# Performance work log

Hardware: AMD Instinct MI355X
Metric: run time of the kernel (lower is better)

Reference implementation:

```python
import jax, jax.numpy as jnp
import numpy as np

B, S, E = 8, 2048, 768
N, H = 12, 64
INIT = 0.02
IGNORE = -100000.0


def setup_inputs() -> dict:
    key = jax.random.key(0)
    ks = jax.random.split(key, 5)
    return {
        "normalized_resid_pre": jax.random.normal(ks[0], (B, S, E), jnp.float32),
        "W_Q": jax.random.normal(ks[1], (N, E, H), jnp.float32) * INIT,
        "W_K": jax.random.normal(ks[2], (N, E, H), jnp.float32) * INIT,
        "W_V": jax.random.normal(ks[3], (N, E, H), jnp.float32) * INIT,
        "W_O": jax.random.normal(ks[4], (N, H, E), jnp.float32) * INIT,
        "b_Q": jnp.zeros((N, H), jnp.float32),
        "b_K": jnp.zeros((N, H), jnp.float32),
        "b_V": jnp.zeros((N, H), jnp.float32),
        "b_O": jnp.zeros((E,), jnp.float32),
    }


def reference(normalized_resid_pre, W_Q, W_K, W_V, W_O, b_Q, b_K, b_V, b_O):
    x = normalized_resid_pre
    b, s, e = x.shape
    d_head = W_Q.shape[-1]
    q = jnp.einsum('bse,neh->bsnh', x, W_Q) + b_Q  # [b, sq, n, h]
    k = jnp.einsum('bse,neh->bsnh', x, W_K) + b_K
    v = jnp.einsum('bse,neh->bsnh', x, W_V) + b_V
    scores = jnp.einsum('bqnh,bknh->bnqk', q, k) / jnp.sqrt(jnp.float32(d_head))
    mask = jnp.tril(jnp.ones((s, s), jnp.float32))  # [sq, sk]
    masked = mask * scores + (1.0 - mask) * IGNORE
    probs = jax.nn.softmax(masked, axis=-1)
    z = jnp.einsum('bnqk,bknh->bqnh', probs, v)
    # sum over heads of per-head output projection + bias
    out = jnp.einsum('bqnh,nhe->bqe', z, W_O) + b_O
    return out
```

## Files before the change

### kernel.cpp

```cpp
#include <hip/hip_runtime.h>
#include <hip/hip_bf16.h>
#include <stdint.h>


#define B_ 8
#define S_ 2048
#define E_ 768
#define NHEADS 12
#define HD 64
#define BS (B_*S_)
#define NHD (NHEADS*HD)

typedef short bf16x8 __attribute__((ext_vector_type(8)));
typedef short bf16x4 __attribute__((ext_vector_type(4)));
typedef float f32x4  __attribute__((ext_vector_type(4)));
typedef __hip_bfloat16 bf16;

typedef const __attribute__((address_space(1))) char* as1_t;
typedef __attribute__((address_space(3))) char* as3_t;

__device__ __forceinline__ f32x4 mfma16(bf16x8 a, bf16x8 b, f32x4 c) {
    return __builtin_amdgcn_mfma_f32_16x16x32_bf16(a, b, c, 0, 0, 0);
}
__device__ __forceinline__ bf16x8 ld8(const bf16* p) {
    return *reinterpret_cast<const bf16x8*>(p);
}
__device__ __forceinline__ void gload16(const bf16* g, bf16* l) {
    __builtin_amdgcn_global_load_lds((as1_t)g, (as3_t)l, 16, 0, 0);
}
__device__ __forceinline__ bf16x8 pack8(f32x4 a, f32x4 b) {
    union { bf16x8 v; __hip_bfloat162 h[4]; } u;
    u.h[0] = __float22bfloat162_rn(make_float2(a[0], a[1]));
    u.h[1] = __float22bfloat162_rn(make_float2(a[2], a[3]));
    u.h[2] = __float22bfloat162_rn(make_float2(b[0], b[1]));
    u.h[3] = __float22bfloat162_rn(make_float2(b[2], b[3]));
    return u.v;
}

__global__ __launch_bounds__(256) void prep_kernel(
    const float* __restrict__ x,  const float* __restrict__ Wq,
    const float* __restrict__ Wk, const float* __restrict__ Wv,
    const float* __restrict__ Wo,
    bf16* __restrict__ xb,  bf16* __restrict__ WqT, bf16* __restrict__ WkT,
    bf16* __restrict__ WvT, bf16* __restrict__ WoT)
{
    const int tid = blockIdx.x * 256 + threadIdx.x;
    const int nth = gridDim.x * 256;
    for (int i = tid; i < BS*E_; i += nth)
        xb[i] = __float2bfloat16(x[i]);
    for (int i = tid; i < NHD*E_; i += nth) {
        const int c = i / E_;
        const int e = i - c*E_;
        const int n = c >> 6, h = c & 63;
        const int src = (n*E_ + e)*HD + h;
        WqT[i] = __float2bfloat16(Wq[src]);
        WkT[i] = __float2bfloat16(Wk[src]);
        WvT[i] = __float2bfloat16(Wv[src]);
        WoT[e*NHD + c] = __float2bfloat16(Wo[i]);
    }
}


#define FENCE() asm volatile("" ::: "memory")
#define VMCNT7() asm volatile("s_waitcnt vmcnt(7)" ::: "memory")
#define MIN11(x) ((x) < 11 ? (x) : 11)

#define A_ELEM(kh, rg) (((kh)*16 + (rg))*512)
#define B_ELEM(kh, rg) (((kh)*12 + (rg))*512)

#define STG_A(dst, gbase, kt, kh) do {                                            \
    const bf16* _s = (gbase) + (size_t)(l16)*768 + (kt)*64 + (kh)*32 + quad*8;    \
    gload16(_s + (size_t)(w*16)*768,     &(dst)[A_ELEM(kh, w)]);                  \
    gload16(_s + (size_t)((w+8)*16)*768, &(dst)[A_ELEM(kh, w+8)]);                \
} while (0)

#define STG_B(dst, gbase, kt) do {                                                \
    const bf16* _s = (gbase) + (size_t)(l16)*768 + (kt)*64 + quad*8;              \
    const int _k1 = (w < 4) ? 0 : 1;                                              \
    const int _r1 = (w < 4) ? (w + 8) : (w - 4);                                  \
    gload16(_s + (size_t)(w*16)*768,        &(dst)[B_ELEM(0, w)]);                \
    gload16(_s + (size_t)(_r1*16)*768 + _k1*32, &(dst)[B_ELEM(_k1, _r1)]);        \
    gload16(_s + (size_t)((w+4)*16)*768 + 32,   &(dst)[B_ELEM(1, w+4)]);          \
} while (0)

#define PHASE(bufA, bufB, q, LOADB, STAGE, WAIT) do {                             \
    if (LOADB) {                                                                  \
        _Pragma("unroll") for (int n = 0; n < 3; ++n)                             \
        _Pragma("unroll") for (int ks = 0; ks < 2; ++ks)                          \
            bfr[n][ks] = ld8(&(bufB)[((ks)*12 + wn*3 + n)*512 + lane*8]);         \
    }                                                                             \
    bf16x8 afr[2][2];                                                             \
    _Pragma("unroll") for (int m = 0; m < 2; ++m)                                 \
    _Pragma("unroll") for (int ks = 0; ks < 2; ++ks)                              \
        afr[m][ks] = ld8(&(bufA)[((ks)*16 + wm*8 + (q)*2 + m)*512 + lane*8]);     \
    STAGE;                                                                        \
    FENCE(); __builtin_amdgcn_s_barrier(); FENCE();                               \
    asm volatile("s_waitcnt lgkmcnt(0)" ::: "memory");                            \
    __builtin_amdgcn_s_setprio(1);                                                \
    _Pragma("unroll") for (int m = 0; m < 2; ++m)                                 \
    _Pragma("unroll") for (int n = 0; n < 3; ++n)                                 \
    _Pragma("unroll") for (int ks = 0; ks < 2; ++ks)                              \
        acc[(q)*2 + m][n] = mfma16(afr[m][ks], bfr[n][ks], acc[(q)*2 + m][n]);    \
    __builtin_amdgcn_s_setprio(0);                                                \
    WAIT;                                                                         \
    FENCE(); __builtin_amdgcn_s_barrier(); FENCE();                               \
} while (0)

#define ITER8(r0, r1, w2, k0, Ab, Bb)                                             \
    PHASE(r0, sB0, 0, 1, STG_A(w2, Ab, MIN11((k0)+2), 0), (void)0);               \
    PHASE(r0, sB0, 1, 0, STG_A(w2, Ab, MIN11((k0)+2), 1), (void)0);               \
    PHASE(r0, sB0, 2, 0, STG_B(sB0, Bb, MIN11((k0)+2)),   (void)0);               \
    PHASE(r0, sB0, 3, 0, (void)0,                         VMCNT7());              \
    PHASE(r1, sB1, 0, 1, STG_A(r0, Ab, MIN11((k0)+3), 0), (void)0);               \
    PHASE(r1, sB1, 1, 0, STG_A(r0, Ab, MIN11((k0)+3), 1), (void)0);               \
    PHASE(r1, sB1, 2, 0, STG_B(sB1, Bb, MIN11((k0)+3)),   (void)0);               \
    PHASE(r1, sB1, 3, 0, (void)0,                         VMCNT7());

#define GEMM192_BODY(Ab, Bb)                                                      \
    f32x4 acc[8][3];                                                              \
    _Pragma("unroll") for (int mf = 0; mf < 8; ++mf)                              \
    _Pragma("unroll") for (int nf = 0; nf < 3; ++nf)                              \
        acc[mf][nf] = (f32x4){0.f, 0.f, 0.f, 0.f};                                \
    bf16x8 bfr[3][2];                                                             \
    STG_A(sA0, Ab, 0, 0); STG_A(sA0, Ab, 0, 1);                                   \
    STG_B(sB0, Bb, 0);                                                            \
    STG_A(sA1, Ab, 1, 0); STG_A(sA1, Ab, 1, 1);                                   \
    STG_B(sB1, Bb, 1);                                                            \
    VMCNT7();                                                                     \
    FENCE(); __builtin_amdgcn_s_barrier(); FENCE();                               \
    _Pragma("unroll 1")                                                           \
    for (int ii = 0; ii < 2; ++ii) {                                              \
        const int k0 = 6*ii;                                                      \
        ITER8(sA0, sA1, sA2, k0+0, Ab, Bb)                                        \
        ITER8(sA2, sA0, sA1, k0+2, Ab, Bb)                                        \
        ITER8(sA1, sA2, sA0, k0+4, Ab, Bb)                                        \
    }                                                                             \
    asm volatile("s_waitcnt vmcnt(0)" ::: "memory");

__global__ __launch_bounds__(512, 2) void qkv_gemm256(
    const bf16* __restrict__ xb, const bf16* __restrict__ WT,
    const float* __restrict__ bq, const float* __restrict__ bk, const float* __restrict__ bv,
    bf16* __restrict__ Qb, bf16* __restrict__ Kb, bf16* __restrict__ VTb)
{
    __shared__ __align__(16) bf16 sA0[16384];
    __shared__ __align__(16) bf16 sA1[16384];
    __shared__ __align__(16) bf16 sA2[16384];
    __shared__ __align__(16) bf16 sB0[12288];
    __shared__ __align__(16) bf16 sB1[12288];

    const int tm = blockIdx.x, tn = blockIdx.y;
    const int lane = threadIdx.x & 63;
    const int w    = threadIdx.x >> 6;
    const int wm = w >> 2, wn = w & 3;
    const int l16 = lane & 15, quad = lane >> 4;
    const bf16* Ab = xb + (size_t)tm*256*E_;
    const bf16* Bb = WT + (size_t)tn*192*E_;

    GEMM192_BODY(Ab, Bb);

    const int mat = tn >> 2;
    const int cloc0 = (tn & 3)*192 + wn*48;
    const float* bias = (mat==0) ? bq : (mat==1) ? bk : bv;
    const float scale = (mat==0) ? 0.125f * 1.44269504088896340736f : 1.0f;
    bf16* dstQK = (mat==0) ? Qb : Kb;
    #pragma unroll
    for (int nf = 0; nf < 3; ++nf) {
        const int col = cloc0 + nf*16 + l16;
        const int hn = col >> 6, h = col & 63;
        const float bb = bias[col];
        #pragma unroll
        for (int mf = 0; mf < 8; ++mf) {
            const int row = tm*256 + wm*128 + mf*16 + quad*4;
            const int bi = row >> 11;
            const int s  = row & (S_-1);
            if (mat < 2) {
                bf16* d = dstQK + ((size_t)(bi*NHEADS + hn)*S_ + s)*HD + h;
                #pragma unroll
                for (int r = 0; r < 4; ++r)
                    d[(size_t)r*HD] = __float2bfloat16((acc[mf][nf][r] + bb)*scale);
            } else {
                bf16* d = VTb + ((size_t)(bi*NHEADS + hn)*HD + h)*S_ + s;
                union { bf16x4 v; bf16 e[4]; } u;
                #pragma unroll
                for (int r = 0; r < 4; ++r) u.e[r] = __float2bfloat16(acc[mf][nf][r] + bb);
                *reinterpret_cast<bf16x4*>(d) = u.v;
            }
        }
    }
}

__global__ __launch_bounds__(512, 2) void out_gemm256(
    const bf16* __restrict__ Z, const bf16* __restrict__ WoT,
    const float* __restrict__ bo, float* __restrict__ out)
{
    __shared__ __align__(16) bf16 sA0[16384];
    __shared__ __align__(16) bf16 sA1[16384];
    __shared__ __align__(16) bf16 sA2[16384];
    __shared__ __align__(16) bf16 sB0[12288];
    __shared__ __align__(16) bf16 sB1[12288];

    const int tm = blockIdx.x, tn = blockIdx.y;
    const int lane = threadIdx.x & 63;
    const int w    = threadIdx.x >> 6;
    const int wm = w >> 2, wn = w & 3;
    const int l16 = lane & 15, quad = lane >> 4;
    const bf16* Ab = Z   + (size_t)tm*256*NHD;
    const bf16* Bb = WoT + (size_t)tn*192*NHD;

    GEMM192_BODY(Ab, Bb);

    #pragma unroll
    for (int nf = 0; nf < 3; ++nf) {
        const int col = tn*192 + wn*48 + nf*16 + l16;
        const float bb = bo[col];
        #pragma unroll
        for (int mf = 0; mf < 8; ++mf) {
            const int row = tm*256 + wm*128 + mf*16 + quad*4;
            float* d = out + (size_t)row*E_ + col;
            #pragma unroll
            for (int r = 0; r < 4; ++r)
                d[(size_t)r*E_] = acc[mf][nf][r] + bb;
        }
    }
}

__global__ __launch_bounds__(256, 3) void attn_kernel(
    const bf16* __restrict__ Qb, const bf16* __restrict__ Kb,
    const bf16* __restrict__ VTb, bf16* __restrict__ Z)
{
    __shared__ __align__(16) bf16 sK[2][64*64];
    __shared__ __align__(16) bf16 sV[2][64*64];

    const int id = blockIdx.x;
    const int bx = id / 96;
    const int g  = id - bx*96;
    const int hn = g % NHEADS, b = g / NHEADS;
    const int tid  = threadIdx.x;
    const int w    = tid >> 6;
    const int lane = tid & 63;
    const int l16 = lane & 15, quad = lane >> 4;
    const size_t bn = (size_t)b*NHEADS + hn;

    const bf16* Qbase = Qb  + bn*S_*HD;
    const bf16* Kbase = Kb  + bn*S_*HD;
    const bf16* Vbase = VTb + bn*HD*S_;

    const int mA = tid, mB = tid + 256;
    const int rA = mA >> 3, cgA = mA & 7;
    const int rB = mB >> 3, cgB = mB & 7;
    const int slA = (rA*8 + ((cgA + rA + (rA>>3)) & 7)) * 8;
    const int slB = (rB*8 + ((cgB + rB + (rB>>3)) & 7)) * 8;
    const size_t vofA = (size_t)rA*S_ + cgA*8;
    const size_t vofB = (size_t)rB*S_ + cgB*8;

    const int kperm = (l16 >> 2)*8 + (l16 & 3);
    int kidx[2][2][2];
    #pragma unroll
    for (int c=0;c<2;c++)
        #pragma unroll
        for (int bg=0;bg<2;bg++)
            #pragma unroll
            for (int hf=0;hf<2;hf++) {
                const int r = 32*c + 4*bg + kperm;
                const int q = hf*4 + quad;
                kidx[c][bg][hf] = (r*8 + ((q + r + (r>>3)) & 7)) * 8;
            }
    int vidx[4][2];
    #pragma unroll
    for (int ht=0;ht<4;ht++)
        #pragma unroll
        for (int c=0;c<2;c++) {
            const int rho = ht*16 + l16;
            const int q = c*4 + quad;
            vidx[ht][c] = (rho*8 + ((q + rho + (rho>>3)) & 7)) * 8;
        }

    #pragma unroll
    for (int half = 0; half < 2; ++half) {
        const int qblk = half ? (S_/128 - 1 - bx) : bx;
        const int ktb  = 2*qblk + 1;
        const int ktw  = 2*qblk + (w >> 1);
        const int qbase = qblk*128 + w*32;

        bf16x8 bqf[2][2];
        #pragma unroll
        for (int qi=0;qi<2;qi++)
            #pragma unroll
            for (int hf=0;hf<2;hf++)
                bqf[qi][hf] = ld8(Qbase + (size_t)(qbase + qi*16 + l16)*HD + hf*32 + quad*8);

        f32x4 acc[2][4];
        #pragma unroll
        for (int qi=0;qi<2;qi++)
            #pragma unroll
            for (int ht=0;ht<4;ht++) acc[qi][ht] = (f32x4){0.f,0.f,0.f,0.f};
        float lsum[2] = {0.f, 0.f};

        bf16x8 k0 = ld8(Kbase + (size_t)mA*8);
        bf16x8 k1 = ld8(Kbase + (size_t)mB*8);
        bf16x8 v0 = ld8(Vbase + vofA);
        bf16x8 v1 = ld8(Vbase + vofB);
        *reinterpret_cast<bf16x8*>(&sK[0][slA]) = k0;
        *reinterpret_cast<bf16x8*>(&sK[0][slB]) = k1;
        *reinterpret_cast<bf16x8*>(&sV[0][slA]) = v0;
        *reinterpret_cast<bf16x8*>(&sV[0][slB]) = v1;
        __syncthreads();

        for (int kt = 0; kt <= ktb; ++kt) {
            if (kt < ktb) {
                const size_t kt1 = (size_t)(kt+1)*64;
                k0 = ld8(Kbase + kt1*HD + (size_t)mA*8);
                k1 = ld8(Kbase + kt1*HD + (size_t)mB*8);
                v0 = ld8(Vbase + vofA + kt1);
                v1 = ld8(Vbase + vofB + kt1);
            }
            if (kt <= ktw) {
                const bf16* kb = sK[kt & 1];
                const bf16* vb = sV[kt & 1];
                #pragma unroll
                for (int c=0;c<2;c++) {
                    const bf16x8 akA0 = ld8(kb + kidx[c][0][0]);
                    const bf16x8 akA1 = ld8(kb + kidx[c][0][1]);
                    const bf16x8 akB0 = ld8(kb + kidx[c][1][0]);
                    const bf16x8 akB1 = ld8(kb + kidx[c][1][1]);
                    bf16x8 av[4];
                    #pragma unroll
                    for (int ht=0;ht<4;ht++) av[ht] = ld8(vb + vidx[ht][c]);

                    #pragma unroll
                    for (int qi=0;qi<2;qi++) {
                        f32x4 s0 = (f32x4){0.f,0.f,0.f,0.f};
                        s0 = mfma16(akA0, bqf[qi][0], s0);
                        s0 = mfma16(akA1, bqf[qi][1], s0);
                        f32x4 s1 = (f32x4){0.f,0.f,0.f,0.f};
                        s1 = mfma16(akB0, bqf[qi][0], s1);
                        s1 = mfma16(akB1, bqf[qi][1], s1);
                        if (kt == ktw) {
                            const int q  = qbase + qi*16 + l16;
                            const int kb0 = kt*64 + c*32 + quad*8;
                            #pragma unroll
                            for (int r=0;r<4;r++) {
                                s0[r] = (kb0 + r     > q) ? -1e30f : s0[r];
                                s1[r] = (kb0 + 4 + r > q) ? -1e30f : s1[r];
                            }
                        }
                        float ls = 0.f;
                        #pragma unroll
                        for (int r=0;r<4;r++) {
                            s0[r] = __builtin_amdgcn_exp2f(s0[r]);
                            s1[r] = __builtin_amdgcn_exp2f(s1[r]);
                            ls += s0[r] + s1[r];
                        }
                        lsum[qi] += ls;
                        const bf16x8 pf = pack8(s0, s1);
                        #pragma unroll
                        for (int ht=0;ht<4;ht++)
                            acc[qi][ht] = mfma16(av[ht], pf, acc[qi][ht]);
                    }
                }
            }
            if (kt < ktb) {
                const int nb = (kt+1) & 1;
                *reinterpret_cast<bf16x8*>(&sK[nb][slA]) = k0;
                *reinterpret_cast<bf16x8*>(&sK[nb][slB]) = k1;
                *reinterpret_cast<bf16x8*>(&sV[nb][slA]) = v0;
                *reinterpret_cast<bf16x8*>(&sV[nb][slB]) = v1;
            }
            __syncthreads();
        }

        #pragma unroll
        for (int qi=0;qi<2;qi++) {
            float rs = lsum[qi];
            rs += __shfl_xor(rs, 16, 64);
            rs += __shfl_xor(rs, 32, 64);
            const float inv_l = 1.0f / rs;
            const int q = qbase + qi*16 + l16;
            bf16* zp = Z + ((size_t)b*S_ + q)*NHD + (size_t)hn*HD + quad*4;
            #pragma unroll
            for (int ht=0;ht<4;ht++) {
                union { bf16x4 v; bf16 e[4]; } u;
                #pragma unroll
                for (int r=0;r<4;r++) u.e[r] = __float2bfloat16(acc[qi][ht][r] * inv_l);
                *reinterpret_cast<bf16x4*>(zp + ht*16) = u.v;
            }
        }
    }
}

extern "C" void kernel_launch(void* const* d_in, const int* in_sizes, int n_in,
                              void* d_out, int out_size, void* d_ws, size_t ws_size,
                              hipStream_t stream)
{
    const float* x  = (const float*)d_in[0];
    const float* Wq = (const float*)d_in[1];
    const float* Wk = (const float*)d_in[2];
    const float* Wv = (const float*)d_in[3];
    const float* Wo = (const float*)d_in[4];
    const float* bq = (const float*)d_in[5];
    const float* bk = (const float*)d_in[6];
    const float* bv = (const float*)d_in[7];
    const float* bo = (const float*)d_in[8];
    float* out = (float*)d_out;

    char* ws = (char*)d_ws;
    size_t off = 0;
    auto alloc = [&](size_t bytes){ char* p = ws + off; off += (bytes + 255) & ~(size_t)255; return p; };
    bf16* xb  = (bf16*)alloc((size_t)BS*E_*2);
    bf16* WT  = (bf16*)alloc((size_t)3*NHD*E_*2);
    bf16* WoT = (bf16*)alloc((size_t)E_*NHD*2);
    bf16* Qb  = (bf16*)alloc((size_t)BS*NHD*2);
    bf16* Kb  = (bf16*)alloc((size_t)BS*NHD*2);
    bf16* VTb = (bf16*)alloc((size_t)BS*NHD*2);
    bf16* Zb  = (bf16*)alloc((size_t)BS*NHD*2);

    bf16* WqT = WT;
    bf16* WkT = WT + (size_t)NHD*E_;
    bf16* WvT = WT + (size_t)2*NHD*E_;

    prep_kernel<<<4096, 256, 0, stream>>>(x, Wq, Wk, Wv, Wo, xb, WqT, WkT, WvT, WoT);
    qkv_gemm256<<<dim3(BS/256, 12), 512, 0, stream>>>(xb, WT, bq, bk, bv, Qb, Kb, VTb);
    attn_kernel<<<768, 256, 0, stream>>>(Qb, Kb, VTb, Zb);
    out_gemm256<<<dim3(BS/256, E_/192), 512, 0, stream>>>(Zb, WoT, bo, out);
}
```

Before: 232.2 us.

## Prepack x and QKV weights into MFMA fragment layout and drop LDS staging

The prep kernel now writes x and the transposed Q/K/V weights in a pre-swizzled 16x32 fragment layout, using vectorized 8-wide conversions for x. A new QKV GEMM with 128x96 tiles and 256 threads loads MFMA operands straight from global memory into registers, with no LDS staging or barriers. This removes shared-memory traffic and synchronization and raises the block count. In exchange it gives up LDS reuse, so each wave rereads operands from global/L2, and there is no explicit software pipelining to hide load latency.

```diff
diff --git a/kernel.cpp b/kernel.cpp
--- a/kernel.cpp
+++ b/kernel.cpp
@@ -37,29 +37,137 @@
     return u.v;
 }
 
+
 __global__ __launch_bounds__(256) void prep_kernel(
     const float* __restrict__ x,  const float* __restrict__ Wq,
     const float* __restrict__ Wk, const float* __restrict__ Wv,
     const float* __restrict__ Wo,
-    bf16* __restrict__ xb,  bf16* __restrict__ WqT, bf16* __restrict__ WkT,
-    bf16* __restrict__ WvT, bf16* __restrict__ WoT)
+    bf16* __restrict__ xp,  bf16* __restrict__ WTp, bf16* __restrict__ WoT)
 {
     const int tid = blockIdx.x * 256 + threadIdx.x;
     const int nth = gridDim.x * 256;
-    for (int i = tid; i < BS*E_; i += nth)
-        xb[i] = __float2bfloat16(x[i]);
+
+    for (int c = tid; c < BS*E_/8; c += nth) {
+        const int r  = c / 96;
+        const int k8 = (c - r*96) * 8;
+        const float4 f0 = *reinterpret_cast<const float4*>(x + (size_t)r*E_ + k8);
+        const float4 f1 = *reinterpret_cast<const float4*>(x + (size_t)r*E_ + k8 + 4);
+        union { bf16x8 v; __hip_bfloat162 h[4]; } u;
+        u.h[0] = __float22bfloat162_rn(make_float2(f0.x, f0.y));
+        u.h[1] = __float22bfloat162_rn(make_float2(f0.z, f0.w));
+        u.h[2] = __float22bfloat162_rn(make_float2(f1.x, f1.y));
+        u.h[3] = __float22bfloat162_rn(make_float2(f1.z, f1.w));
+        const size_t dst = (size_t)((r>>4)*24 + (k8>>5))*512
+                         + (size_t)((((k8>>3)&3)<<4) + (r&15))*8;
+        *reinterpret_cast<bf16x8*>(xp + dst) = u.v;
+    }
+
+    for (int c2 = tid; c2 < NHD*96; c2 += nth) {
+        const int r  = c2 / 96;
+        const int e8 = (c2 - r*96) * 8;
+        const int n = r >> 6, h = r & 63;
+        const float* sq = Wq + (size_t)(n*E_ + e8)*HD + h;
+        const float* sk = Wk + (size_t)(n*E_ + e8)*HD + h;
+        const float* sv = Wv + (size_t)(n*E_ + e8)*HD + h;
+        union { bf16x8 v; bf16 el[8]; } uq, uk, uv;
+        #pragma unroll
+        for (int j = 0; j < 8; ++j) {
+            uq.el[j] = __float2bfloat16(sq[(size_t)j*HD]);
+            uk.el[j] = __float2bfloat16(sk[(size_t)j*HD]);
+            uv.el[j] = __float2bfloat16(sv[(size_t)j*HD]);
+        }
+        const size_t sub = (size_t)(e8>>5)*512
+                         + (size_t)((((e8>>3)&3)<<4) + (r&15))*8;
+        const size_t rg  = (size_t)(r>>4);
+        *reinterpret_cast<bf16x8*>(WTp + ((0*48 + rg)*24)*512 + sub) = uq.v;
+        *reinterpret_cast<bf16x8*>(WTp + ((1*48 + rg)*24)*512 + sub) = uk.v;
+        *reinterpret_cast<bf16x8*>(WTp + ((2*48 + rg)*24)*512 + sub) = uv.v;
+    }
+
     for (int i = tid; i < NHD*E_; i += nth) {
-        const int c = i / E_;
-        const int e = i - c*E_;
-        const int n = c >> 6, h = c & 63;
-        const int src = (n*E_ + e)*HD + h;
-        WqT[i] = __float2bfloat16(Wq[src]);
-        WkT[i] = __float2bfloat16(Wk[src]);
-        WvT[i] = __float2bfloat16(Wv[src]);
-        WoT[e*NHD + c] = __float2bfloat16(Wo[i]);
-    }
-}
-
+        const int cc = i / E_;
+        const int e  = i - cc*E_;
+        WoT[(size_t)e*NHD + cc] = __float2bfloat16(Wo[i]);
+    }
+}
+
+__global__ __launch_bounds__(256, 3) void qkv_gemm_p(
+    const bf16* __restrict__ xp, const bf16* __restrict__ WTp,
+    const float* __restrict__ bq, const float* __restrict__ bk, const float* __restrict__ bv,
+    bf16* __restrict__ Qb, bf16* __restrict__ Kb, bf16* __restrict__ VTb)
+{
+    const int tm = blockIdx.x, tn = blockIdx.y;
+    const int lane = threadIdx.x & 63;
+    const int w    = threadIdx.x >> 6;
+    const int wm = w >> 1, wn = w & 1;
+    const int l16 = lane & 15, quad = lane >> 4;
+    const bf16* Abase = xp  + (size_t)(tm*8 + wm*4)*24*512 + lane*8;
+    const bf16* Bbase = WTp + (size_t)(tn*6 + wn*3)*24*512 + lane*8;
+
+    f32x4 acc[4][3];
+    #pragma unroll
+    for (int mf = 0; mf < 4; ++mf)
+        #pragma unroll
+        for (int nf = 0; nf < 3; ++nf)
+            acc[mf][nf] = (f32x4){0.f, 0.f, 0.f, 0.f};
+
+    #pragma unroll
+    for (int kt = 0; kt < 12; ++kt) {
+        bf16x8 af[4][2], bfr[3][2];
+        #pragma unroll
+        for (int m = 0; m < 2; ++m)
+            #pragma unroll
+            for (int ks = 0; ks < 2; ++ks)
+                af[m][ks] = ld8(Abase + ((size_t)m*24 + kt*2 + ks)*512);
+        #pragma unroll
+        for (int n = 0; n < 3; ++n)
+            #pragma unroll
+            for (int ks = 0; ks < 2; ++ks)
+                bfr[n][ks] = ld8(Bbase + ((size_t)n*24 + kt*2 + ks)*512);
+        #pragma unroll
+        for (int m = 2; m < 4; ++m)
+            #pragma unroll
+            for (int ks = 0; ks < 2; ++ks)
+                af[m][ks] = ld8(Abase + ((size_t)m*24 + kt*2 + ks)*512);
+        #pragma unroll
+        for (int ks = 0; ks < 2; ++ks)
+            #pragma unroll
+            for (int m = 0; m < 4; ++m)
+                #pragma unroll
+                for (int n = 0; n < 3; ++n)
+                    acc[m][n] = mfma16(af[m][ks], bfr[n][ks], acc[m][n]);
+    }
+
+    const int mat = tn >> 3;
+    const int cloc0 = (tn & 7)*96 + wn*48;
+    const float* bias = (mat==0) ? bq : (mat==1) ? bk : bv;
+    const float scale = (mat==0) ? 0.125f * 1.44269504088896340736f : 1.0f;
+    bf16* dstQK = (mat==0) ? Qb : Kb;
+    #pragma unroll
+    for (int nf = 0; nf < 3; ++nf) {
+        const int col = cloc0 + nf*16 + l16;
+        const int hn = col >> 6, h = col & 63;
+        const float bb = bias[col];
+        #pragma unroll
+        for (int mf = 0; mf < 4; ++mf) {
+            const int row = tm*128 + wm*64 + mf*16 + quad*4;
+            const int bi = row >> 11;
+            const int s  = row & (S_-1);
+            if (mat < 2) {
+                bf16* d = dstQK + ((size_t)(bi*NHEADS + hn)*S_ + s)*HD + h;
+                #pragma unroll
+                for (int r = 0; r < 4; ++r)
+                    d[(size_t)r*HD] = __float2bfloat16((acc[mf][nf][r] + bb)*scale);
+            } else {
+                bf16* d = VTb + ((size_t)(bi*NHEADS + hn)*HD + h)*S_ + s;
+                union { bf16x4 v; bf16 e[4]; } u;
+                #pragma unroll
+                for (int r = 0; r < 4; ++r) u.e[r] = __float2bfloat16(acc[mf][nf][r] + bb);
+                *reinterpret_cast<bf16x4*>(d) = u.v;
+            }
+        }
+    }
+}
 
 #define FENCE() asm volatile("" ::: "memory")
 #define VMCNT7() asm volatile("s_waitcnt vmcnt(7)" ::: "memory")
@@ -136,58 +244,6 @@
         ITER8(sA1, sA2, sA0, k0+4, Ab, Bb)                                        \
     }                                                                             \
     asm volatile("s_waitcnt vmcnt(0)" ::: "memory");
-
-__global__ __launch_bounds__(512, 2) void qkv_gemm256(
-    const bf16* __restrict__ xb, const bf16* __restrict__ WT,
-    const float* __restrict__ bq, const float* __restrict__ bk, const float* __restrict__ bv,
-    bf16* __restrict__ Qb, bf16* __restrict__ Kb, bf16* __restrict__ VTb)
-{
-    __shared__ __align__(16) bf16 sA0[16384];
-    __shared__ __align__(16) bf16 sA1[16384];
-    __shared__ __align__(16) bf16 sA2[16384];
-    __shared__ __align__(16) bf16 sB0[12288];
-    __shared__ __align__(16) bf16 sB1[12288];
-
-    const int tm = blockIdx.x, tn = blockIdx.y;
-    const int lane = threadIdx.x & 63;
-    const int w    = threadIdx.x >> 6;
-    const int wm = w >> 2, wn = w & 3;
-    const int l16 = lane & 15, quad = lane >> 4;
-    const bf16* Ab = xb + (size_t)tm*256*E_;
-    const bf16* Bb = WT + (size_t)tn*192*E_;
-
-    GEMM192_BODY(Ab, Bb);
-
-    const int mat = tn >> 2;
-    const int cloc0 = (tn & 3)*192 + wn*48;
-    const float* bias = (mat==0) ? bq : (mat==1) ? bk : bv;
-    const float scale = (mat==0) ? 0.125f * 1.44269504088896340736f : 1.0f;
-    bf16* dstQK = (mat==0) ? Qb : Kb;
-    #pragma unroll
-    for (int nf = 0; nf < 3; ++nf) {
-        const int col = cloc0 + nf*16 + l16;
-        const int hn = col >> 6, h = col & 63;
-        const float bb = bias[col];
-        #pragma unroll
-        for (int mf = 0; mf < 8; ++mf) {
-            const int row = tm*256 + wm*128 + mf*16 + quad*4;
-            const int bi = row >> 11;
-            const int s  = row & (S_-1);
-            if (mat < 2) {
-                bf16* d = dstQK + ((size_t)(bi*NHEADS + hn)*S_ + s)*HD + h;
-                #pragma unroll
-                for (int r = 0; r < 4; ++r)
-                    d[(size_t)r*HD] = __float2bfloat16((acc[mf][nf][r] + bb)*scale);
-            } else {
-                bf16* d = VTb + ((size_t)(bi*NHEADS + hn)*HD + h)*S_ + s;
-                union { bf16x4 v; bf16 e[4]; } u;
-                #pragma unroll
-                for (int r = 0; r < 4; ++r) u.e[r] = __float2bfloat16(acc[mf][nf][r] + bb);
-                *reinterpret_cast<bf16x4*>(d) = u.v;
-            }
-        }
-    }
-}
 
 __global__ __launch_bounds__(512, 2) void out_gemm256(
     const bf16* __restrict__ Z, const bf16* __restrict__ WoT,
@@ -406,20 +462,16 @@
     char* ws = (char*)d_ws;
     size_t off = 0;
     auto alloc = [&](size_t bytes){ char* p = ws + off; off += (bytes + 255) & ~(size_t)255; return p; };
-    bf16* xb  = (bf16*)alloc((size_t)BS*E_*2);
-    bf16* WT  = (bf16*)alloc((size_t)3*NHD*E_*2);
+    bf16* xp  = (bf16*)alloc((size_t)BS*E_*2);
+    bf16* WTp = (bf16*)alloc((size_t)3*NHD*E_*2);
     bf16* WoT = (bf16*)alloc((size_t)E_*NHD*2);
     bf16* Qb  = (bf16*)alloc((size_t)BS*NHD*2);
     bf16* Kb  = (bf16*)alloc((size_t)BS*NHD*2);
     bf16* VTb = (bf16*)alloc((size_t)BS*NHD*2);
     bf16* Zb  = (bf16*)alloc((size_t)BS*NHD*2);
 
-    bf16* WqT = WT;
-    bf16* WkT = WT + (size_t)NHD*E_;
-    bf16* WvT = WT + (size_t)2*NHD*E_;
-
-    prep_kernel<<<4096, 256, 0, stream>>>(x, Wq, Wk, Wv, Wo, xb, WqT, WkT, WvT, WoT);
-    qkv_gemm256<<<dim3(BS/256, 12), 512, 0, stream>>>(xb, WT, bq, bk, bv, Qb, Kb, VTb);
+    prep_kernel<<<4096, 256, 0, stream>>>(x, Wq, Wk, Wv, Wo, xp, WTp, WoT);
+    qkv_gemm_p<<<dim3(BS/128, 24), 256, 0, stream>>>(xp, WTp, bq, bk, bv, Qb, Kb, VTb);
     attn_kernel<<<768, 256, 0, stream>>>(Qb, Kb, VTb, Zb);
     out_gemm256<<<dim3(BS/256, E_/192), 512, 0, stream>>>(Zb, WoT, bo, out);
 }
```

After: 258.2 us. 1.11x slower.
